# Performance work log

Hardware: AMD Instinct MI355X
Metric: run time of the kernel (lower is better)

## Reference

```python
import jax, jax.numpy as jnp
import numpy as np


def setup_inputs() -> dict:
    key = jax.random.key(0)
    k1, k2 = jax.random.split(key)
    B, N, D = 4, 2048, 1024
    x = jax.random.normal(k1, (B, N, D), dtype=jnp.float32)
    # torch nn.Linear weight shape [out_features, in_features] = [3D, D]
    w_qkv = jax.random.normal(k2, (3 * D, D), dtype=jnp.float32) * (D ** -0.5)
    return {"x": x, "w_qkv": w_qkv}


def reference(x, w_qkv):
    D = x.shape[-1]
    scale = D ** -0.5
    qkv = jnp.einsum('bnd,ed->bne', x, w_qkv)  # [B, N, 3D]
    q, k, v = jnp.split(qkv, 3, axis=-1)
    scores = jnp.einsum('bnd,bmd->bnm', q, k) * scale  # [B, N, N]
    attn = jax.nn.softmax(scores, axis=-1)
    return jnp.einsum('bnm,bmd->bnd', attn, v)
```

## Files before the change

### kernel.cpp

```cpp
#include <hip/hip_runtime.h>
#include <hip/hip_bf16.h>


typedef __bf16 bf16x8 __attribute__((ext_vector_type(8)));
typedef float f32x4 __attribute__((ext_vector_type(4)));

__device__ __forceinline__ void store_out(float* p, float v) { *p = v; }
__device__ __forceinline__ void store_out(__hip_bfloat16* p, float v) { *p = __float2bfloat16(v); }

__global__ __launch_bounds__(256)
void cast_f32_bf16(const float* __restrict__ in, __hip_bfloat16* __restrict__ out, int n4) {
  for (int i = blockIdx.x * blockDim.x + threadIdx.x; i < n4; i += gridDim.x * blockDim.x) {
    float4 v = ((const float4*)in)[i];
    __hip_bfloat16 b0 = __float2bfloat16(v.x), b1 = __float2bfloat16(v.y),
                   b2 = __float2bfloat16(v.z), b3 = __float2bfloat16(v.w);
    ushort4 o;
    o.x = *(unsigned short*)&b0; o.y = *(unsigned short*)&b1;
    o.z = *(unsigned short*)&b2; o.w = *(unsigned short*)&b3;
    ((ushort4*)out)[i] = o;
  }
}


#define PHASE(P, CB, PF, K0N)                                                          \
  {                                                                                    \
    bf16x8 a00 = frag(CB, 0, wm * 128 + P * 32 +  0, 0);                               \
    bf16x8 a01 = frag(CB, 0, wm * 128 + P * 32 +  0, 1);                               \
    bf16x8 a10 = frag(CB, 0, wm * 128 + P * 32 + 16, 0);                               \
    bf16x8 a11 = frag(CB, 0, wm * 128 + P * 32 + 16, 1);                               \
    if (P == 0) {                                                                      \
      _Pragma("unroll") for (int j = 0; j < 4; ++j) {                                  \
        bfr[j][0] = frag(CB, 1, wn * 64 + j * 16, 0);                                  \
        bfr[j][1] = frag(CB, 1, wn * 64 + j * 16, 1);                                  \
      }                                                                                \
    }                                                                                  \
    if (PF) {                                                                          \
      if (P == 0) { stage(CB ^ 1, 0,   0, K0N); stage(CB ^ 1, 0, 128, K0N); }          \
      if (P == 1) { stage(CB ^ 1, 1,   0, K0N); stage(CB ^ 1, 1,  64, K0N); }          \
      if (P == 2) { stage(CB ^ 1, 1, 128, K0N); stage(CB ^ 1, 1, 192, K0N); }          \
      if (P == 3) { stage(CB ^ 1, 0,  64, K0N); stage(CB ^ 1, 0, 192, K0N); }          \
    }                                                                                  \
    if (P == 0) asm volatile("s_waitcnt lgkmcnt(8)" ::: "memory");                     \
    if (P == 1) {                                                                      \
      if (PF) asm volatile("s_waitcnt vmcnt(4)" ::: "memory");                         \
      else    asm volatile("s_waitcnt vmcnt(0)" ::: "memory");                         \
    }                                                                                  \
    if (P == 3) { if (PF) asm volatile("s_waitcnt vmcnt(2)" ::: "memory"); }           \
    __builtin_amdgcn_s_barrier();                                                      \
    asm volatile("s_waitcnt lgkmcnt(0)" ::: "memory");                                 \
    __builtin_amdgcn_sched_barrier(0);                                                 \
    __builtin_amdgcn_s_setprio(1);                                                     \
    _Pragma("unroll") for (int j = 0; j < 4; ++j) {                                    \
      acc[P * 2 + 0][j] = __builtin_amdgcn_mfma_f32_16x16x32_bf16(a00, bfr[j][0], acc[P * 2 + 0][j], 0, 0, 0); \
      acc[P * 2 + 0][j] = __builtin_amdgcn_mfma_f32_16x16x32_bf16(a01, bfr[j][1], acc[P * 2 + 0][j], 0, 0, 0); \
      acc[P * 2 + 1][j] = __builtin_amdgcn_mfma_f32_16x16x32_bf16(a10, bfr[j][0], acc[P * 2 + 1][j], 0, 0, 0); \
      acc[P * 2 + 1][j] = __builtin_amdgcn_mfma_f32_16x16x32_bf16(a11, bfr[j][1], acc[P * 2 + 1][j], 0, 0, 0); \
    }                                                                                  \
    __builtin_amdgcn_s_setprio(0);                                                     \
    __builtin_amdgcn_s_barrier();                                                      \
  }

template <typename OutT>
__global__ __launch_bounds__(512, 2)
void gemm256(const __hip_bfloat16* __restrict__ A, int lda, long sA,
             const __hip_bfloat16* __restrict__ B, int ldb, long sB,
             OutT* __restrict__ C, int ldc, long sC,
             int K, float cscale) {
  extern __shared__ char smem[];
  const int tid = threadIdx.x, lane = tid & 63, wid = tid >> 6;
  const int wm = wid >> 2, wn = wid & 3;
  A += (long)blockIdx.z * sA; B += (long)blockIdx.z * sB; C += (long)blockIdx.z * sC;
  const long bm = (long)blockIdx.x * 256, bn = (long)blockIdx.y * 256;
  const int laneOff = (lane & 15) * 64 + (((lane >> 4) * 16) ^ ((lane & 8) ? 32 : 0));
  const int sRowA = (wid >> 1) * 16 + (lane >> 2);
  const int sKs   = wid & 1;
  const int sCol  = ((lane & 3) * 8) ^ ((lane & 32) ? 16 : 0);
  const int nt = K >> 6;

  auto stage = [&](int cbuf, int reg , int row0, int k0) {
    const __hip_bfloat16* g =
        reg ? (B + (bn + row0 + sRowA) * (long)ldb + k0 + sKs * 32 + sCol)
            : (A + (bm + row0 + sRowA) * (long)lda + k0 + sKs * 32 + sCol);
    char* dst = smem + cbuf * 65536 + reg * 32768 + ((row0 >> 4) * 2 + wid) * 1024;
    __builtin_amdgcn_global_load_lds((const __attribute__((address_space(1))) void*)g,
                                     (__attribute__((address_space(3))) void*)dst, 16, 0, 0);
  };
  auto frag = [&](int cbuf, int reg, int R, int ks) -> bf16x8 {
    return *(const bf16x8*)(smem + cbuf * 65536 + reg * 32768 +
                            ((R >> 4) * 2 + ks) * 1024 + laneOff);
  };

  f32x4 acc[8][4] = {};
  bf16x8 bfr[4][2];

  stage(0, 0,   0, 0); stage(0, 0, 128, 0);
  stage(0, 1,   0, 0); stage(0, 1,  64, 0);
  stage(0, 1, 128, 0); stage(0, 1, 192, 0);
  stage(0, 0,  64, 0); stage(0, 0, 192, 0);
  asm volatile("s_waitcnt vmcnt(2)" ::: "memory");
  __builtin_amdgcn_s_barrier();

  for (int t = 0; t < nt; t += 2) {
    {
      const int k0n = (t + 1) << 6;
      PHASE(0, 0, true, k0n) PHASE(1, 0, true, k0n)
      PHASE(2, 0, true, k0n) PHASE(3, 0, true, k0n)
    }
    {
      const bool pf = (t + 2) < nt;
      const int k0n = (t + 2) << 6;
      PHASE(0, 1, pf, k0n) PHASE(1, 1, pf, k0n)
      PHASE(2, 1, pf, k0n) PHASE(3, 1, pf, k0n)
    }
  }

  const int r0 = (lane >> 4) * 4, cn = lane & 15;
#pragma unroll
  for (int rf = 0; rf < 8; ++rf)
#pragma unroll
    for (int j = 0; j < 4; ++j) {
      long row = bm + wm * 128 + rf * 16 + r0;
      long col = bn + wn * 64 + j * 16 + cn;
#pragma unroll
      for (int jj = 0; jj < 4; ++jj)
        store_out(&C[(row + jj) * (long)ldc + col], acc[rf][j][jj] * cscale);
    }
}

__global__ __launch_bounds__(256)
void transpose_v(const __hip_bfloat16* __restrict__ qkv, __hip_bfloat16* __restrict__ Vt) {
  __shared__ __hip_bfloat16 tile[32][33];
  const int b = blockIdx.z;
  const __hip_bfloat16* V = qkv + (size_t)b * 2048 * 3072 + 2048;
  __hip_bfloat16* vt = Vt + (size_t)b * 1024 * 2048;
  const int tx = threadIdx.x & 31, ty = threadIdx.x >> 5;
  const int m0 = blockIdx.x * 32, d0 = blockIdx.y * 32;
#pragma unroll
  for (int i = 0; i < 32; i += 8)
    tile[ty + i][tx] = V[(size_t)(m0 + ty + i) * 3072 + d0 + tx];
  __syncthreads();
#pragma unroll
  for (int i = 0; i < 32; i += 8)
    vt[(size_t)(d0 + ty + i) * 2048 + m0 + tx] = tile[tx][ty + i];
}

__global__ __launch_bounds__(256)
void softmax_rows(float* __restrict__ S) {
  float* row = S + (size_t)blockIdx.x * 2048;
  const int t = threadIdx.x, lane = t & 63, wid = t >> 6;
  float4 v0 = ((const float4*)row)[t];
  float4 v1 = ((const float4*)row)[256 + t];
  float vals[8] = {v0.x, v0.y, v0.z, v0.w, v1.x, v1.y, v1.z, v1.w};
  float m = vals[0];
#pragma unroll
  for (int i = 1; i < 8; ++i) m = fmaxf(m, vals[i]);
#pragma unroll
  for (int o = 32; o; o >>= 1) m = fmaxf(m, __shfl_xor(m, o));
  __shared__ float red[4];
  if (lane == 0) red[wid] = m;
  __syncthreads();
  m = fmaxf(fmaxf(red[0], red[1]), fmaxf(red[2], red[3]));
  __syncthreads();
  float p[8], s = 0.f;
#pragma unroll
  for (int i = 0; i < 8; ++i) { p[i] = __expf(vals[i] - m); s += p[i]; }
#pragma unroll
  for (int o = 32; o; o >>= 1) s += __shfl_xor(s, o);
  if (lane == 0) red[wid] = s;
  __syncthreads();
  s = red[0] + red[1] + red[2] + red[3];
  const float inv = 1.0f / s;
  __hip_bfloat16 b[8];
#pragma unroll
  for (int i = 0; i < 8; ++i) b[i] = __float2bfloat16(p[i] * inv);
  ushort4 o0, o1;
  o0.x = *(unsigned short*)&b[0]; o0.y = *(unsigned short*)&b[1];
  o0.z = *(unsigned short*)&b[2]; o0.w = *(unsigned short*)&b[3];
  o1.x = *(unsigned short*)&b[4]; o1.y = *(unsigned short*)&b[5];
  o1.z = *(unsigned short*)&b[6]; o1.w = *(unsigned short*)&b[7];
  unsigned short* prow = (unsigned short*)row;
  ((ushort4*)prow)[t] = o0;
  ((ushort4*)prow)[256 + t] = o1;
}

extern "C" void kernel_launch(void* const* d_in, const int* in_sizes, int n_in,
                              void* d_out, int out_size, void* d_ws, size_t ws_size,
                              hipStream_t stream) {
  const float* x = (const float*)d_in[0];
  const float* w = (const float*)d_in[1];
  float* out = (float*)d_out;
  char* ws = (char*)d_ws;

  __hip_bfloat16* xb  = (__hip_bfloat16*)ws;
  __hip_bfloat16* wb  = (__hip_bfloat16*)(ws + 16777216);
  float*          S   = (float*)ws;
  __hip_bfloat16* qkv = (__hip_bfloat16*)(ws + 67108864);
  __hip_bfloat16* Vt  = (__hip_bfloat16*)(ws + 117440512);

  cast_f32_bf16<<<1024, 256, 0, stream>>>(x, xb, (4 * 2048 * 1024) / 4);
  cast_f32_bf16<<<512, 256, 0, stream>>>(w, wb, (3072 * 1024) / 4);

  gemm256<__hip_bfloat16><<<dim3(32, 12, 1), 512, 131072, stream>>>(
      xb, 1024, 0L, wb, 1024, 0L, qkv, 3072, 0L, 1024, 1.0f);

  transpose_v<<<dim3(64, 32, 4), 256, 0, stream>>>(qkv, Vt);

  gemm256<float><<<dim3(8, 8, 4), 512, 131072, stream>>>(
      qkv, 3072, (long)2048 * 3072, qkv + 1024, 3072, (long)2048 * 3072,
      S, 2048, (long)2048 * 2048, 1024, 0.03125f);

  softmax_rows<<<8192, 256, 0, stream>>>(S);

  gemm256<float><<<dim3(8, 4, 4), 512, 131072, stream>>>(
      (const __hip_bfloat16*)S, 4096, (long)2048 * 4096,
      Vt, 2048, (long)1024 * 2048,
      out, 1024, (long)2048 * 1024, 2048, 1.0f);
}
```

Before: 267.9 us.

## Template GEMM on M-fragments; use 128-row tiles for PV GEMM and simplify prefetch waits

Parameterizes the GEMM kernel on the number of M fragments so the tile can be 128x256 instead of 256x256. The final attention-times-V GEMM uses the smaller tile, doubling its grid from 128 to 256 blocks to fill more CUs, and its LDS request drops to 96KB. The prefetch schedule also changes: all next-buffer loads are issued in phase 0 and a full vmcnt(0) wait happens at phase 3, replacing the staggered partial waits. That simpler scheme may expose more load latency in the two GEMMs that keep the 256-row tile.

```diff
diff --git a/kernel.cpp b/kernel.cpp
--- a/kernel.cpp
+++ b/kernel.cpp
@@ -7,6 +7,8 @@
 
 __device__ __forceinline__ void store_out(float* p, float v) { *p = v; }
 __device__ __forceinline__ void store_out(__hip_bfloat16* p, float v) { *p = __float2bfloat16(v); }
+
+#define MFMA16(a, b, c) __builtin_amdgcn_mfma_f32_16x16x32_bf16(a, b, c, 0, 0, 0)
 
 __global__ __launch_bounds__(256)
 void cast_f32_bf16(const float* __restrict__ in, __hip_bfloat16* __restrict__ out, int n4) {
@@ -24,80 +26,77 @@
 
 #define PHASE(P, CB, PF, K0N)                                                          \
   {                                                                                    \
-    bf16x8 a00 = frag(CB, 0, wm * 128 + P * 32 +  0, 0);                               \
-    bf16x8 a01 = frag(CB, 0, wm * 128 + P * 32 +  0, 1);                               \
-    bf16x8 a10 = frag(CB, 0, wm * 128 + P * 32 + 16, 0);                               \
-    bf16x8 a11 = frag(CB, 0, wm * 128 + P * 32 + 16, 1);                               \
+    bf16x8 af[MFRAGS][2];                                                              \
+    _Pragma("unroll") for (int mf = 0; mf < MFRAGS; ++mf) {                            \
+      af[mf][0] = frag(CB, 0, wm * (MFRAGS * 64) + (P * MFRAGS + mf) * 16, 0);         \
+      af[mf][1] = frag(CB, 0, wm * (MFRAGS * 64) + (P * MFRAGS + mf) * 16, 1);         \
+    }                                                                                  \
     if (P == 0) {                                                                      \
       _Pragma("unroll") for (int j = 0; j < 4; ++j) {                                  \
         bfr[j][0] = frag(CB, 1, wn * 64 + j * 16, 0);                                  \
         bfr[j][1] = frag(CB, 1, wn * 64 + j * 16, 1);                                  \
       }                                                                                \
+      if (PF) stage_all(CB ^ 1, K0N);                                                  \
+      asm volatile("s_waitcnt lgkmcnt(8)" ::: "memory");                               \
     }                                                                                  \
-    if (PF) {                                                                          \
-      if (P == 0) { stage(CB ^ 1, 0,   0, K0N); stage(CB ^ 1, 0, 128, K0N); }          \
-      if (P == 1) { stage(CB ^ 1, 1,   0, K0N); stage(CB ^ 1, 1,  64, K0N); }          \
-      if (P == 2) { stage(CB ^ 1, 1, 128, K0N); stage(CB ^ 1, 1, 192, K0N); }          \
-      if (P == 3) { stage(CB ^ 1, 0,  64, K0N); stage(CB ^ 1, 0, 192, K0N); }          \
-    }                                                                                  \
-    if (P == 0) asm volatile("s_waitcnt lgkmcnt(8)" ::: "memory");                     \
-    if (P == 1) {                                                                      \
-      if (PF) asm volatile("s_waitcnt vmcnt(4)" ::: "memory");                         \
-      else    asm volatile("s_waitcnt vmcnt(0)" ::: "memory");                         \
-    }                                                                                  \
-    if (P == 3) { if (PF) asm volatile("s_waitcnt vmcnt(2)" ::: "memory"); }           \
     __builtin_amdgcn_s_barrier();                                                      \
     asm volatile("s_waitcnt lgkmcnt(0)" ::: "memory");                                 \
     __builtin_amdgcn_sched_barrier(0);                                                 \
     __builtin_amdgcn_s_setprio(1);                                                     \
-    _Pragma("unroll") for (int j = 0; j < 4; ++j) {                                    \
-      acc[P * 2 + 0][j] = __builtin_amdgcn_mfma_f32_16x16x32_bf16(a00, bfr[j][0], acc[P * 2 + 0][j], 0, 0, 0); \
-      acc[P * 2 + 0][j] = __builtin_amdgcn_mfma_f32_16x16x32_bf16(a01, bfr[j][1], acc[P * 2 + 0][j], 0, 0, 0); \
-      acc[P * 2 + 1][j] = __builtin_amdgcn_mfma_f32_16x16x32_bf16(a10, bfr[j][0], acc[P * 2 + 1][j], 0, 0, 0); \
-      acc[P * 2 + 1][j] = __builtin_amdgcn_mfma_f32_16x16x32_bf16(a11, bfr[j][1], acc[P * 2 + 1][j], 0, 0, 0); \
-    }                                                                                  \
+    _Pragma("unroll") for (int j = 0; j < 4; ++j)                                      \
+      _Pragma("unroll") for (int mf = 0; mf < MFRAGS; ++mf) {                          \
+        acc[P * MFRAGS + mf][j] = MFMA16(af[mf][0], bfr[j][0], acc[P * MFRAGS + mf][j]); \
+        acc[P * MFRAGS + mf][j] = MFMA16(af[mf][1], bfr[j][1], acc[P * MFRAGS + mf][j]); \
+      }                                                                                \
     __builtin_amdgcn_s_setprio(0);                                                     \
+    if (P == 3) asm volatile("s_waitcnt vmcnt(0)" ::: "memory");                       \
     __builtin_amdgcn_s_barrier();                                                      \
   }
 
-template <typename OutT>
+template <typename OutT, int MFRAGS>
 __global__ __launch_bounds__(512, 2)
 void gemm256(const __hip_bfloat16* __restrict__ A, int lda, long sA,
              const __hip_bfloat16* __restrict__ B, int ldb, long sB,
              OutT* __restrict__ C, int ldc, long sC,
              int K, float cscale) {
+  constexpr int BM = MFRAGS * 128;
+  constexpr int ABYTES = BM * 64 * 2;
+  constexpr int BUFSZ = ABYTES + 32768;
   extern __shared__ char smem[];
   const int tid = threadIdx.x, lane = tid & 63, wid = tid >> 6;
   const int wm = wid >> 2, wn = wid & 3;
   A += (long)blockIdx.z * sA; B += (long)blockIdx.z * sB; C += (long)blockIdx.z * sC;
-  const long bm = (long)blockIdx.x * 256, bn = (long)blockIdx.y * 256;
+  const long bm = (long)blockIdx.x * BM, bn = (long)blockIdx.y * 256;
   const int laneOff = (lane & 15) * 64 + (((lane >> 4) * 16) ^ ((lane & 8) ? 32 : 0));
   const int sRowA = (wid >> 1) * 16 + (lane >> 2);
-  const int sKs   = wid & 1;
-  const int sCol  = ((lane & 3) * 8) ^ ((lane & 32) ? 16 : 0);
+  const int sKs = wid & 1;
+  const int sCol = ((lane & 3) * 8) ^ ((lane & 32) ? 16 : 0);
   const int nt = K >> 6;
 
   auto stage = [&](int cbuf, int reg , int row0, int k0) {
     const __hip_bfloat16* g =
         reg ? (B + (bn + row0 + sRowA) * (long)ldb + k0 + sKs * 32 + sCol)
             : (A + (bm + row0 + sRowA) * (long)lda + k0 + sKs * 32 + sCol);
-    char* dst = smem + cbuf * 65536 + reg * 32768 + ((row0 >> 4) * 2 + wid) * 1024;
+    char* dst = smem + cbuf * BUFSZ + (reg ? ABYTES : 0) + ((row0 >> 4) * 2 + wid) * 1024;
     __builtin_amdgcn_global_load_lds((const __attribute__((address_space(1))) void*)g,
                                      (__attribute__((address_space(3))) void*)dst, 16, 0, 0);
   };
+  auto stage_all = [&](int cbuf, int k0) {
+    stage(cbuf, 0, 0, k0); stage(cbuf, 0, 64, k0);
+    if (MFRAGS == 2) { stage(cbuf, 0, 128, k0); stage(cbuf, 0, 192, k0); }
+    stage(cbuf, 1, 0, k0); stage(cbuf, 1, 64, k0);
+    stage(cbuf, 1, 128, k0); stage(cbuf, 1, 192, k0);
+  };
   auto frag = [&](int cbuf, int reg, int R, int ks) -> bf16x8 {
-    return *(const bf16x8*)(smem + cbuf * 65536 + reg * 32768 +
+    return *(const bf16x8*)(smem + cbuf * BUFSZ + (reg ? ABYTES : 0) +
                             ((R >> 4) * 2 + ks) * 1024 + laneOff);
   };
 
-  f32x4 acc[8][4] = {};
+  f32x4 acc[MFRAGS * 4][4] = {};
   bf16x8 bfr[4][2];
 
-  stage(0, 0,   0, 0); stage(0, 0, 128, 0);
-  stage(0, 1,   0, 0); stage(0, 1,  64, 0);
-  stage(0, 1, 128, 0); stage(0, 1, 192, 0);
-  stage(0, 0,  64, 0); stage(0, 0, 192, 0);
-  asm volatile("s_waitcnt vmcnt(2)" ::: "memory");
+  stage_all(0, 0);
+  asm volatile("s_waitcnt vmcnt(0)" ::: "memory");
   __builtin_amdgcn_s_barrier();
 
   for (int t = 0; t < nt; t += 2) {
@@ -116,10 +115,10 @@
 
   const int r0 = (lane >> 4) * 4, cn = lane & 15;
 #pragma unroll
-  for (int rf = 0; rf < 8; ++rf)
+  for (int rf = 0; rf < MFRAGS * 4; ++rf)
 #pragma unroll
     for (int j = 0; j < 4; ++j) {
-      long row = bm + wm * 128 + rf * 16 + r0;
+      long row = bm + wm * (MFRAGS * 64) + rf * 16 + r0;
       long col = bn + wn * 64 + j * 16 + cn;
 #pragma unroll
       for (int jj = 0; jj < 4; ++jj)
@@ -200,18 +199,18 @@
   cast_f32_bf16<<<1024, 256, 0, stream>>>(x, xb, (4 * 2048 * 1024) / 4);
   cast_f32_bf16<<<512, 256, 0, stream>>>(w, wb, (3072 * 1024) / 4);
 
-  gemm256<__hip_bfloat16><<<dim3(32, 12, 1), 512, 131072, stream>>>(
+  gemm256<__hip_bfloat16, 2><<<dim3(32, 12, 1), 512, 131072, stream>>>(
       xb, 1024, 0L, wb, 1024, 0L, qkv, 3072, 0L, 1024, 1.0f);
 
   transpose_v<<<dim3(64, 32, 4), 256, 0, stream>>>(qkv, Vt);
 
-  gemm256<float><<<dim3(8, 8, 4), 512, 131072, stream>>>(
+  gemm256<float, 2><<<dim3(8, 8, 4), 512, 131072, stream>>>(
       qkv, 3072, (long)2048 * 3072, qkv + 1024, 3072, (long)2048 * 3072,
       S, 2048, (long)2048 * 2048, 1024, 0.03125f);
 
   softmax_rows<<<8192, 256, 0, stream>>>(S);
 
-  gemm256<float><<<dim3(8, 4, 4), 512, 131072, stream>>>(
+  gemm256<float, 1><<<dim3(16, 4, 4), 512, 98304, stream>>>(
       (const __hip_bfloat16*)S, 4096, (long)2048 * 4096,
       Vt, 2048, (long)1024 * 2048,
       out, 1024, (long)2048 * 1024, 2048, 1.0f);
```

Result: faster. 260.9 us (-2.6%).
